# Kernel tuning notes

Measured on AMD Instinct MI355X. Metric: run time of the kernel, lower is better.

## Reference

```python
import jax, jax.numpy as jnp
import numpy as np

N = 100_000      # atoms
E = 1_600_000    # edges (avg degree 16)
B = 50           # graphs in batch
H = 128          # hidden dim
R = 50           # num radial features (emb(0.0, 6.0, 50))
MAXZ = 100
CUTOFF = 6.0
L = 3            # interaction layers (ext[1..6])


def setup_inputs() -> dict:
    key = jax.random.key(0)
    ks = jax.random.split(key, 16)
    z = jax.random.randint(ks[0], (N,), 0, MAXZ)
    pos = jax.random.normal(ks[1], (N, 3), dtype=jnp.float32) * 3.0
    cell = jnp.eye(3, dtype=jnp.float32)[None] * 10.0 + 0.1 * jax.random.normal(ks[2], (B, 3, 3), dtype=jnp.float32)
    edge_index = jax.random.randint(ks[3], (2, E), 0, N)
    cell_offsets = jax.random.randint(ks[4], (E, 3), -1, 2)  # {-1,0,1}
    edge_batch = jax.random.randint(ks[5], (E,), 0, B)
    # learned parameters
    atom_emb = jax.random.normal(ks[6], (MAXZ, H), dtype=jnp.float32) * 0.1
    dist_table = jax.random.normal(ks[7], (R, R), dtype=jnp.float32) * 0.1  # dist_emb embedding table
    s_e = 1.0 / np.sqrt(2 * H + R)
    s_h = 1.0 / np.sqrt(H)
    We = jax.random.normal(ks[8], (L, 2 * H + R, H), dtype=jnp.float32) * s_e
    be = jnp.zeros((L, H), dtype=jnp.float32)
    Wv = jax.random.normal(ks[9], (L, H, H), dtype=jnp.float32) * s_h
    bv = jnp.zeros((L, H), dtype=jnp.float32)
    Wh = jax.random.normal(ks[10], (H, H), dtype=jnp.float32) * s_h
    bh = jnp.zeros((H,), dtype=jnp.float32)
    return dict(z=z, pos=pos, cell=cell, edge_index=edge_index,
                cell_offsets=cell_offsets, edge_batch=edge_batch,
                atom_emb=atom_emb, dist_table=dist_table,
                We=We, be=be, Wv=Wv, bv=bv, Wh=Wh, bh=bh)


def reference(z, pos, cell, edge_index, cell_offsets, edge_batch,
              atom_emb, dist_table, We, be, Wv, bv, Wh, bh):
    row, col = edge_index[0], edge_index[1]
    # get_pbc_distances: offsets = cell_offsets @ per-edge cell
    off = jnp.einsum('ek,ekl->el', cell_offsets.astype(jnp.float32), cell[edge_batch])  # [E,3]
    vec = pos[row] - pos[col] + off
    dist = jnp.sqrt(jnp.sum(vec * vec, axis=-1))  # [E]
    # dist_emb(dist.to(long)): integer-cast distance indexes the embedding table
    demb = dist_table[jnp.clip(dist.astype(jnp.int32), 0, R - 1)]  # [E,R]
    env = 0.5 * (jnp.cos(jnp.pi * jnp.clip(dist, 0.0, CUTOFF) / CUTOFF) + 1.0)  # cosine cutoff [E]
    v = atom_emb[z]  # ext[0]: atom embedding [N,H]
    for i in range(L):
        # ext[2i+1]: edge layer — gather endpoints, concat with radial features
        m = jnp.concatenate([v[row], v[col], demb], axis=-1)  # [E, 2H+R]
        e = jax.nn.silu(m @ We[i] + be[i]) * env[:, None]     # [E, H]
        # ext[2i+2]: node layer — scatter-sum messages to destination nodes
        agg = jax.ops.segment_sum(e, col, num_segments=N)     # [N, H]
        v = v + jax.nn.silu(agg @ Wv[i] + bv[i])
    v = v @ Wh + bh  # head
    return (v, pos, dist)
```

## Files before the change

kernel.cpp:

```cpp
#include <hip/hip_runtime.h>
#include <hip/hip_bf16.h>

#define HID 128
#define RR 50
#define NLAY 3
#define CBSH 9
#define CBSZ 512
#define CPAD (CBSZ * 3)
#define ACHUNK 8192

typedef __attribute__((ext_vector_type(8))) short short8;
typedef __attribute__((ext_vector_type(4))) float f32x4;
typedef __attribute__((ext_vector_type(2))) float f32x2;

static __device__ __forceinline__ unsigned short f2bf(float x) {
    unsigned int b = __builtin_bit_cast(unsigned int, x);
    b = b + 0x7FFFu + ((b >> 16) & 1u);
    return (unsigned short)(b >> 16);
}
static __device__ __forceinline__ float bf2f(unsigned int u) {
    return __builtin_bit_cast(float, u << 16);
}
static __device__ __forceinline__ f32x2 bfpair(unsigned u) {
    f32x2 r;
    r.x = __builtin_bit_cast(float, u << 16);
    r.y = __builtin_bit_cast(float, u & 0xffff0000u);
    return r;
}
static __device__ __forceinline__ float silu_f(float x) {
    float e = __expf(-x);
    return x * __builtin_amdgcn_rcpf(1.0f + e);
}

__global__ __launch_bounds__(256) void k_geom(
    const int* __restrict__ ei, const int* __restrict__ co,
    const int* __restrict__ eb, const float* __restrict__ cell,
    const float* __restrict__ pos, float* __restrict__ dist_out,
    int2* __restrict__ rec, int* __restrict__ ccol,
    float* __restrict__ out_pos, int* __restrict__ gb,
    int N3, int E, int nCB)
{
    __shared__ int lc[1024];
    int tid = threadIdx.x;
    for (int i = tid; i < 1024; i += 256) lc[i] = 0;
    __syncthreads();
    int e = blockIdx.x * 256 + tid;
    if (e < N3) out_pos[e] = pos[e];
    if (e < E) {
        int r = ei[e], c = ei[E + e], b = eb[e];
        float c0 = (float)co[3*e], c1 = (float)co[3*e+1], c2 = (float)co[3*e+2];
        const float* cb = cell + b * 9;
        float v0 = pos[3*r+0] - pos[3*c+0] + c0*cb[0] + c1*cb[3] + c2*cb[6];
        float v1 = pos[3*r+1] - pos[3*c+1] + c0*cb[1] + c1*cb[4] + c2*cb[7];
        float v2 = pos[3*r+2] - pos[3*c+2] + c0*cb[2] + c1*cb[5] + c2*cb[8];
        float d = sqrtf(v0*v0 + v1*v1 + v2*v2);
        dist_out[e] = d;
        bool keep = d < 6.0f;
        ccol[e] = keep ? c : -1;
        if (keep) {
            int di = (int)d;
            di = di < 0 ? 0 : (di > RR - 1 ? RR - 1 : di);
            float envv = 0.5f * (cosf(d * (3.14159265358979323846f / 6.0f)) + 1.0f);
            rec[e] = make_int2((r << 8) | di, __builtin_bit_cast(int, envv));
            atomicAdd(&lc[((unsigned)c) >> CBSH], 1);
        }
    }
    __syncthreads();
    for (int i = tid; i < nCB; i += 256)
        if (lc[i]) atomicAdd(&gb[i], lc[i]);
}

__global__ __launch_bounds__(256) void k_projz(
    const int* __restrict__ z, const float* __restrict__ emb,
    const unsigned short* __restrict__ P12t,
    unsigned short* __restrict__ v, unsigned short* __restrict__ P1,
    unsigned short* __restrict__ P2, int N)
{
    int gid = blockIdx.x * 256 + threadIdx.x;
    if (gid >= N * 16) return;
    int n = gid >> 4, c4 = gid & 15;
    int zz = z[n];
    const float4* ep = (const float4*)(emb + (size_t)zz * HID) + c4 * 2;
    float4 a = ep[0], b = ep[1];
    uint4 u;
    u.x = ((unsigned)f2bf(a.y) << 16) | f2bf(a.x);
    u.y = ((unsigned)f2bf(a.w) << 16) | f2bf(a.z);
    u.z = ((unsigned)f2bf(b.y) << 16) | f2bf(b.x);
    u.w = ((unsigned)f2bf(b.w) << 16) | f2bf(b.z);
    *(uint4*)(v + (size_t)n * HID + c4 * 8) = u;
    uint4 t1 = *(const uint4*)(P12t + (size_t)zz * 256 + c4 * 8);
    uint4 t2 = *(const uint4*)(P12t + (size_t)zz * 256 + 128 + c4 * 8);
    *(uint4*)(P1 + (size_t)n * HID + c4 * 8) = t1;
    *(uint4*)(P2 + (size_t)n * HID + c4 * 8) = t2;
}

__global__ __launch_bounds__(256) void k_wprep(
    const float* __restrict__ We, const float* __restrict__ Wv,
    const float* __restrict__ Wh, const float* __restrict__ dt,
    const float* __restrict__ be, const float* __restrict__ emb,
    unsigned short* __restrict__ WvP, unsigned short* __restrict__ WcP,
    unsigned short* __restrict__ WhP, unsigned short* __restrict__ TbP,
    unsigned short* __restrict__ P12t)
{
    int blk = blockIdx.x;
    if (blk < 640) {
        int t = blk * 256 + threadIdx.x;
        int j = t & 7, l = (t >> 3) & 63, s = (t >> 9) & 3;
        int ln = l & 15, g = l >> 4;
        int k = s * 32 + g * 4 + (j & 3) + ((j >> 2) << 4);
        if (t < 3 * 16384) {
            int i = t >> 14; int nt = (t >> 11) & 7;
            WvP[t] = f2bf(Wv[(size_t)i * 16384 + k * HID + nt * 16 + ln]);
        } else if (t < 3 * 16384 + 3 * 32768) {
            int u = t - 3 * 16384; int i = u >> 15; int nt = (u >> 11) & 15;
            int col = nt * 16 + ln;
            float val = (col < HID) ? We[(size_t)i * 306 * HID + k * HID + col]
                                    : We[(size_t)i * 306 * HID + (HID + k) * HID + (col - HID)];
            WcP[u] = f2bf(val);
        } else {
            int u = t - 3 * 16384 - 3 * 32768; int nt = (u >> 11) & 7;
            WhP[u] = f2bf(Wh[k * HID + nt * 16 + ln]);
        }
    } else if (blk < 640 + NLAY * RR) {
        if (threadIdx.x >= HID) return;
        int row = blk - 640;
        int i = row / RR, r = row % RR;
        int c = threadIdx.x;
        float s = be[i * HID + c];
        const float* w = We + (size_t)i * 306 * HID + 256 * HID + c;
        const float* dr = dt + r * RR;
        for (int k = 0; k < RR; ++k) s += dr[k] * w[k * HID];
        TbP[(i * RR + r) * HID + c] = f2bf(s);
    } else {
        int zz = blk - 640 - NLAY * RR;
        int c = threadIdx.x;
        int cm = c & 127, half = c >> 7;
        const float* er = emb + (size_t)zz * HID;
        const float* w = We + (size_t)(half * 128) * HID + cm;
        float s = 0.f;
        #pragma unroll 8
        for (int k = 0; k < 128; ++k) s += er[k] * w[k * HID];
        P12t[(size_t)zz * 256 + c] = f2bf(s);
    }
}

__global__ __launch_bounds__(256) void k_scanA(
    const int* __restrict__ gb, int* __restrict__ gbase,
    int* __restrict__ gcur, int nCB)
{
    __shared__ int ps[256];
    __shared__ int carry;
    int t = threadIdx.x;
    if (t == 0) carry = 0;
    __syncthreads();
    for (int base = 0; base < nCB; base += 256) {
        int v = (base + t < nCB) ? gb[base + t] : 0;
        ps[t] = v; __syncthreads();
        for (int d = 1; d < 256; d <<= 1) {
            int x = (t >= d) ? ps[t - d] : 0;
            __syncthreads();
            ps[t] += x;
            __syncthreads();
        }
        int excl = carry + ps[t] - v;
        if (base + t < nCB) { gbase[base + t] = excl; gcur[base + t] = excl; }
        __syncthreads();
        if (t == 0) carry += ps[255];
        __syncthreads();
    }
    if (t == 0) gbase[nCB] = carry;
}

__global__ __launch_bounds__(256) void k_splitA(
    const int* __restrict__ col, const int2* __restrict__ rec,
    int* __restrict__ gcur, int2* __restrict__ binned,
    int* __restrict__ bcol, int E, int nCB)
{
    __shared__ int lc[1024];
    __shared__ int lres[1024];
    int tid = threadIdx.x;
    for (int i = tid; i < nCB; i += 256) lc[i] = 0;
    __syncthreads();
    int base = blockIdx.x * ACHUNK;
    int end = base + ACHUNK; if (end > E) end = E;
    for (int e = base + tid; e < end; e += 256) {
        int c = col[e];
        if (c >= 0) atomicAdd(&lc[((unsigned)c) >> CBSH], 1);
    }
    __syncthreads();
    for (int i = tid; i < nCB; i += 256) {
        lres[i] = lc[i] ? atomicAdd(&gcur[i], lc[i]) : 0;
        lc[i] = 0;
    }
    __syncthreads();
    for (int e = base + tid; e < end; e += 256) {
        int c = col[e];
        if (c < 0) continue;
        int b = ((unsigned)c) >> CBSH;
        int rank = atomicAdd(&lc[b], 1);
        int p = lres[b] + rank;
        binned[p] = rec[e];
        bcol[p] = c;
    }
}

__global__ __launch_bounds__(256) void k_sortB(
    const int2* __restrict__ binned, const int* __restrict__ bcol,
    const int* __restrict__ gbase, int2* __restrict__ meta,
    int2* __restrict__ noff, int N)
{
    __shared__ int lcnt[CBSZ], lcur[CBSZ], pscan[CBSZ];
    __shared__ int wsum[64];
    const int b = blockIdx.x;
    const int tid = threadIdx.x;
    const int s = gbase[b], e = gbase[b + 1];
    const int mbase = s + b * CPAD;
    for (int i = tid; i < CBSZ; i += 256) { lcnt[i] = 0; lcur[i] = 0; }
    __syncthreads();
    for (int t = s + tid; t < e; t += 256)
        atomicAdd(&lcnt[bcol[t] & (CBSZ - 1)], 1);
    __syncthreads();
    if (tid < 64) {
        int ssum = 0;
        #pragma unroll
        for (int k = 0; k < 8; ++k) {
            int idx = tid * 8 + k;
            int pc = (lcnt[idx] + 3) & ~3;
            pscan[idx] = ssum;
            ssum += pc;
        }
        wsum[tid] = ssum;
    }
    __syncthreads();
    if (tid == 0) {
        int c = 0;
        for (int i = 0; i < 64; ++i) { int t = wsum[i]; wsum[i] = c; c += t; }
    }
    __syncthreads();
    if (tid < 64) {
        #pragma unroll
        for (int k = 0; k < 8; ++k) pscan[tid * 8 + k] += wsum[tid];
    }
    __syncthreads();
    for (int i = tid; i < CBSZ; i += 256) {
        int node = (b << CBSH) + i;
        if (node < N) {
            noff[node] = make_int2(mbase + pscan[i], lcnt[i]);
            int pb = mbase + pscan[i] + lcnt[i];
            int pads = ((lcnt[i] + 3) & ~3) - lcnt[i];
            for (int k = 0; k < pads; ++k) meta[pb + k] = make_int2(0, 0);
        }
    }
    __syncthreads();
    for (int t = s + tid; t < e; t += 256) {
        int local = bcol[t] & (CBSZ - 1);
        int rank = atomicAdd(&lcur[local], 1);
        meta[mbase + pscan[local] + rank] = binned[t];
    }
}

#define PLD(M) (*(const unsigned*)(P1b + (unsigned)((((unsigned)(M).x) & 0xFFFFFF00u) | lane4)))
#define TLDG(M) (*(const unsigned*)(Tb_ + (((((unsigned)(M).x) & 255u) << 8) | lane4)))

#define EP(GG, TBU, MM)                                                       \
    {                                                                         \
        f32x2 xx = bfpair(GG) + (bfpair(TBU) + p2v);                          \
        f32x2 nx = xx * -1.442695041f;                                        \
        f32x2 ee;                                                             \
        ee.x = __builtin_amdgcn_exp2f(nx.x);                                  \
        ee.y = __builtin_amdgcn_exp2f(nx.y);                                  \
        f32x2 dd = ee + 1.0f;                                                 \
        f32x2 rr;                                                             \
        rr.x = __builtin_amdgcn_rcpf(dd.x);                                   \
        rr.y = __builtin_amdgcn_rcpf(dd.y);                                   \
        f32x2 sl = xx * rr;                                                   \
        float evf = __builtin_bit_cast(float, (MM).y);                        \
        av += sl * evf;                                                       \
    }

static __device__ __forceinline__ short8 ldfrag(const unsigned short* A, int r, int s, int g) {
    const char* p = (const char*)(A + r * 136) + s * 64 + g * 8;
    uint2 lo = *(const uint2*)p;
    uint2 hi = *(const uint2*)(p + 32);
    uint4 u; u.x = lo.x; u.y = lo.y; u.z = hi.x; u.w = hi.y;
    return __builtin_bit_cast(short8, u);
}

template<int NT2, bool FINAL>
__global__ __launch_bounds__(512) void k_layer(
    const unsigned short* __restrict__ P1,
    const unsigned short* __restrict__ P2,
    const unsigned short* __restrict__ TbBf,
    const int2* __restrict__ meta,
    const int2* __restrict__ noff,
    const unsigned short* __restrict__ B1p,
    const float* __restrict__ b1,
    unsigned short* __restrict__ v,
    const unsigned short* __restrict__ B2p,
    const float* __restrict__ b2,
    unsigned short* __restrict__ P1d,
    unsigned short* __restrict__ P2d,
    float* __restrict__ outd, int N)
{
    __shared__ __align__(16) unsigned short SHB[2 * 32 * 136];
    unsigned short* SH  = SHB;
    unsigned short* SHV = SHB + 32 * 136;
    const int tid = threadIdx.x;
    const int node0 = blockIdx.x * 32;
    const int w = tid >> 6, l = tid & 63, g = (l >> 4) & 3, ln = l & 15;
    const int lane = l;
    const unsigned lane4 = 4u * (unsigned)lane;

    {
        int r = tid >> 4, c = tid & 15;
        uint4 y4 = make_uint4(0, 0, 0, 0);
        if (node0 + r < N) y4 = *(const uint4*)(v + (size_t)(node0 + r) * HID + c * 8);
        *(uint4*)(SHV + r * 136 + c * 8) = y4;
    }

    {
        const char* P1b = (const char*)P1;
        const char* Tb_ = (const char*)TbBf;
        const int r0 = w << 2;
        int2 ni = make_int2(0, 0);
        {
            int pn = node0 + r0 + lane;
            if (lane < 4 && pn < N) ni = noff[pn];
        }
        #pragma unroll 1
        for (int i = 0; i < 4; ++i) {
            int r = r0 + i;
            unsigned* outp = (unsigned*)(SH + r * 136 + 2 * lane);
            int n = __builtin_amdgcn_readlane(ni.y, i);
            if (n == 0) { *outp = 0u; continue; }
            int s = __builtin_amdgcn_readlane(ni.x, i);
            int node = node0 + r;
            unsigned p2u = *(const unsigned*)(P2 + (size_t)node * HID + 2 * lane);
            n = (n + 3) & ~3;
            f32x2 p2v = bfpair(p2u);
            f32x2 av; av.x = 0.f; av.y = 0.f;
            const int2* mp = meta + s;
            int2 m0 = mp[0], m1 = mp[1], m2 = mp[2], m3 = mp[3];
            unsigned g0 = PLD(m0), g1 = PLD(m1), g2 = PLD(m2), g3 = PLD(m3);
            for (int t = 0; t < n; t += 4) {
                int2 n0 = mp[t + 4], n1 = mp[t + 5], n2 = mp[t + 6], n3 = mp[t + 7];
                unsigned h0 = PLD(n0), h1 = PLD(n1), h2 = PLD(n2), h3 = PLD(n3);
                unsigned t0 = TLDG(m0), t1 = TLDG(m1), t2 = TLDG(m2), t3 = TLDG(m3);
                EP(g0, t0, m0) EP(g1, t1, m1) EP(g2, t2, m2) EP(g3, t3, m3)
                m0 = n0; m1 = n1; m2 = n2; m3 = n3;
                g0 = h0; g1 = h1; g2 = h2; g3 = h3;
            }
            *outp = (((unsigned)f2bf(av.y)) << 16) | (unsigned)f2bf(av.x);
        }
    }

    {
        short8 bf1[4];
        #pragma unroll
        for (int s = 0; s < 4; ++s)
            bf1[s] = *(const short8*)(B1p + ((w * 4 + s) * 64 + l) * 8);
        __syncthreads();
        f32x4 acc[2] = {};
        #pragma unroll
        for (int s = 0; s < 4; ++s)
            #pragma unroll
            for (int mt = 0; mt < 2; ++mt) {
                short8 af = ldfrag(SH, 16 * mt + ln, s, g);
                acc[mt] = __builtin_amdgcn_mfma_f32_16x16x32_bf16(af, bf1[s], acc[mt], 0, 0, 0);
            }
        __syncthreads();
        float bvc = b1[16 * w + ln];
        #pragma unroll
        for (int mt = 0; mt < 2; ++mt) {
            int col = 16 * w + ln;
            #pragma unroll
            for (int j = 0; j < 4; ++j) {
                int r = 16 * mt + 4 * g + j;
                float y = silu_f(acc[mt][j] + bvc);
                float vn = bf2f((unsigned)SHV[r * 136 + col]) + y;
                SH[r * 136 + col] = f2bf(vn);
            }
        }
        __syncthreads();
        if (!FINAL) {
            int r = tid >> 4, c = tid & 15;
            if (node0 + r < N)
                *(uint4*)(v + (size_t)(node0 + r) * HID + c * 8) =
                    *(const uint4*)(SH + r * 136 + c * 8);
        }
    }

    constexpr int NTW = NT2 / 8;
    short8 bf2[NTW][4];
    #pragma unroll
    for (int nt = 0; nt < NTW; ++nt)
        #pragma unroll
        for (int s = 0; s < 4; ++s)
            bf2[nt][s] = *(const short8*)(B2p + (((w * NTW + nt) * 4 + s) * 64 + l) * 8);
    f32x4 acc2[2][NTW] = {};
    #pragma unroll
    for (int s = 0; s < 4; ++s)
        #pragma unroll
        for (int mt = 0; mt < 2; ++mt) {
            short8 af = ldfrag(SH, 16 * mt + ln, s, g);
            #pragma unroll
            for (int nt = 0; nt < NTW; ++nt)
                acc2[mt][nt] = __builtin_amdgcn_mfma_f32_16x16x32_bf16(af, bf2[nt][s], acc2[mt][nt], 0, 0, 0);
        }
    __syncthreads();
    if (FINAL) {
        float* fst = (float*)SHB;
        int col = w * 16 + ln;
        float bb = b2[col];
        #pragma unroll
        for (int mt = 0; mt < 2; ++mt)
            #pragma unroll
            for (int j = 0; j < 4; ++j) {
                int r = 16 * mt + 4 * g + j;
                fst[r * 132 + col] = acc2[mt][0][j] + bb;
            }
        __syncthreads();
        #pragma unroll
        for (int i = 0; i < 2; ++i) {
            int u = tid + 512 * i, r = u >> 5, cg = u & 31;
            if (node0 + r < N)
                *(float4*)(outd + (size_t)(node0 + r) * HID + cg * 4) =
                    *(const float4*)(fst + r * 132 + cg * 4);
        }
    } else {
        #pragma unroll
        for (int nt = 0; nt < NTW; ++nt) {
            int gidx = w * NTW + nt;
            int colm = (gidx * 16 + ln) & 127;
            unsigned short* dst = (gidx < 8) ? SHV : SH;
            #pragma unroll
            for (int mt = 0; mt < 2; ++mt)
                #pragma unroll
                for (int j = 0; j < 4; ++j) {
                    int r = 16 * mt + 4 * g + j;
                    dst[r * 136 + colm] = f2bf(acc2[mt][nt][j]);
                }
        }
        __syncthreads();
        {
            int r = tid >> 4, cg = tid & 15;
            if (node0 + r < N) {
                *(uint4*)(P1d + (size_t)(node0 + r) * HID + cg * 8) =
                    *(const uint4*)(SHV + r * 136 + cg * 8);
                *(uint4*)(P2d + (size_t)(node0 + r) * HID + cg * 8) =
                    *(const uint4*)(SH + r * 136 + cg * 8);
            }
        }
    }
}

extern "C" void kernel_launch(void* const* d_in, const int* in_sizes, int n_in,
                              void* d_out, int out_size, void* d_ws, size_t ws_size,
                              hipStream_t stream)
{
    const int*   z    = (const int*)d_in[0];
    const float* pos  = (const float*)d_in[1];
    const float* cell = (const float*)d_in[2];
    const int*   ei   = (const int*)d_in[3];
    const int*   co   = (const int*)d_in[4];
    const int*   eb   = (const int*)d_in[5];
    const float* emb  = (const float*)d_in[6];
    const float* dt   = (const float*)d_in[7];
    const float* We   = (const float*)d_in[8];
    const float* be   = (const float*)d_in[9];
    const float* Wv   = (const float*)d_in[10];
    const float* bv   = (const float*)d_in[11];
    const float* Wh   = (const float*)d_in[12];
    const float* bh   = (const float*)d_in[13];

    const int N = in_sizes[0];
    const int E = in_sizes[5];
    const int MAXZ = in_sizes[6] / HID;
    const int nCB = (N + CBSZ - 1) >> CBSH;
    const size_t metaN = (size_t)E + (size_t)nCB * CPAD + 32;

    char* p = (char*)d_ws;
    unsigned short* v    = (unsigned short*)p;  p += (size_t)N * HID * 2;
    unsigned short* P1a  = (unsigned short*)p;  p += (size_t)N * HID * 2;
    unsigned short* P1b  = (unsigned short*)p;  p += (size_t)N * HID * 2;
    unsigned short* P2   = (unsigned short*)p;  p += (size_t)N * HID * 2;
    int2*  meta  = (int2*)p;                    p += metaN * 8;
    int2*  noff  = (int2*)p;                    p += (size_t)N * 8;
    int*   gb    = (int*)p;                     p += (size_t)(nCB + 1) * 4;
    int*   gbase = (int*)p;                     p += (size_t)(nCB + 1) * 4;
    int*   gcur  = (int*)p;                     p += (size_t)(nCB + 1) * 4;
    unsigned short* TbP = (unsigned short*)p;   p += (size_t)NLAY * RR * HID * 2;
    unsigned short* WvP = (unsigned short*)p;   p += (size_t)3 * 16384 * 2;
    unsigned short* WcP = (unsigned short*)p;   p += (size_t)3 * 32768 * 2;
    unsigned short* WhP = (unsigned short*)p;   p += (size_t)16384 * 2;
    unsigned short* P12t = (unsigned short*)p;  p += (size_t)MAXZ * 256 * 2;

    int2* rec    = (int2*)P1a;
    int2* binned = (int2*)((char*)P1a + (size_t)E * 8);
    int*  ccol   = (int*)P2;
    int*  bcol   = (int*)((char*)P2 + (size_t)E * 4);

    float* out_v    = (float*)d_out;
    float* out_pos  = out_v + (size_t)N * HID;
    float* out_dist = out_pos + (size_t)N * 3;

    const int nlayer = (N + 31) / 32;
    const int nblkA = (E + ACHUNK - 1) / ACHUNK;
    const int N3 = N * 3;
    int ngeom = (E + 255) / 256;
    if ((N3 + 255) / 256 > ngeom) ngeom = (N3 + 255) / 256;

    hipMemsetAsync(gb, 0, (size_t)(nCB + 1) * 4, stream);
    hipMemsetAsync(meta, 0, metaN * 8, stream);
    k_geom<<<ngeom, 256, 0, stream>>>(ei, co, eb, cell, pos, out_dist, rec, ccol,
                                      out_pos, gb, N3, E, nCB);
    k_scanA<<<1, 256, 0, stream>>>(gb, gbase, gcur, nCB);
    k_splitA<<<nblkA, 256, 0, stream>>>(ccol, rec, gcur, binned, bcol, E, nCB);
    k_sortB<<<nCB, 256, 0, stream>>>(binned, bcol, gbase, meta, noff, N);

    k_wprep<<<640 + NLAY * RR + MAXZ, 256, 0, stream>>>(
        We, Wv, Wh, dt, be, emb, WvP, WcP, WhP, TbP, P12t);

    k_projz<<<(N * 16 + 255) / 256, 256, 0, stream>>>(z, emb, P12t, v, P1a, P2, N);

    unsigned short* Pin  = P1a;
    unsigned short* Pout = P1b;
    for (int i = 0; i < NLAY; ++i) {
        if (i < NLAY - 1) {
            k_layer<16, false><<<nlayer, 512, 0, stream>>>(
                Pin, P2, TbP + (size_t)i * RR * HID, meta, noff,
                WvP + (size_t)i * 16384, bv + (size_t)i * HID, v,
                WcP + (size_t)(i + 1) * 32768, nullptr, Pout, P2, nullptr, N);
        } else {
            k_layer<8, true><<<nlayer, 512, 0, stream>>>(
                Pin, P2, TbP + (size_t)i * RR * HID, meta, noff,
                WvP + (size_t)i * 16384, bv + (size_t)i * HID, v,
                WhP, bh, nullptr, nullptr, out_v, N);
        }
        unsigned short* t = Pin; Pin = Pout; Pout = t;
    }
}
```

Before: 246.7 us.

## Fuse atom-embedding init into first layer and use global atomics in geometry

The first layer kernel now builds the bf16 node state straight from the atom embedding table and reads the P2 projection from the per-species table. k_projz therefore writes only P1, and the N×H v and P2 initial writes and their reads go away. k_geom drops its shared-memory bucket histogram and does one global atomicAdd per kept edge, which removes two block barriers but adds heavy global atomic contention on about 200 counters.

Measured after the change: 257.6 us. 4.4% more time.

```diff
diff --git a/kernel.cpp b/kernel.cpp
--- a/kernel.cpp
+++ b/kernel.cpp
@@ -37,61 +37,40 @@
     const int* __restrict__ eb, const float* __restrict__ cell,
     const float* __restrict__ pos, float* __restrict__ dist_out,
     int2* __restrict__ rec, int* __restrict__ ccol,
-    float* __restrict__ out_pos, int* __restrict__ gb,
-    int N3, int E, int nCB)
-{
-    __shared__ int lc[1024];
-    int tid = threadIdx.x;
-    for (int i = tid; i < 1024; i += 256) lc[i] = 0;
-    __syncthreads();
-    int e = blockIdx.x * 256 + tid;
+    float* __restrict__ out_pos, int* __restrict__ gb, int N3, int E)
+{
+    int e = blockIdx.x * 256 + threadIdx.x;
     if (e < N3) out_pos[e] = pos[e];
-    if (e < E) {
-        int r = ei[e], c = ei[E + e], b = eb[e];
-        float c0 = (float)co[3*e], c1 = (float)co[3*e+1], c2 = (float)co[3*e+2];
-        const float* cb = cell + b * 9;
-        float v0 = pos[3*r+0] - pos[3*c+0] + c0*cb[0] + c1*cb[3] + c2*cb[6];
-        float v1 = pos[3*r+1] - pos[3*c+1] + c0*cb[1] + c1*cb[4] + c2*cb[7];
-        float v2 = pos[3*r+2] - pos[3*c+2] + c0*cb[2] + c1*cb[5] + c2*cb[8];
-        float d = sqrtf(v0*v0 + v1*v1 + v2*v2);
-        dist_out[e] = d;
-        bool keep = d < 6.0f;
-        ccol[e] = keep ? c : -1;
-        if (keep) {
-            int di = (int)d;
-            di = di < 0 ? 0 : (di > RR - 1 ? RR - 1 : di);
-            float envv = 0.5f * (cosf(d * (3.14159265358979323846f / 6.0f)) + 1.0f);
-            rec[e] = make_int2((r << 8) | di, __builtin_bit_cast(int, envv));
-            atomicAdd(&lc[((unsigned)c) >> CBSH], 1);
-        }
-    }
-    __syncthreads();
-    for (int i = tid; i < nCB; i += 256)
-        if (lc[i]) atomicAdd(&gb[i], lc[i]);
+    if (e >= E) return;
+    int r = ei[e], c = ei[E + e], b = eb[e];
+    float c0 = (float)co[3*e], c1 = (float)co[3*e+1], c2 = (float)co[3*e+2];
+    const float* cb = cell + b * 9;
+    float v0 = pos[3*r+0] - pos[3*c+0] + c0*cb[0] + c1*cb[3] + c2*cb[6];
+    float v1 = pos[3*r+1] - pos[3*c+1] + c0*cb[1] + c1*cb[4] + c2*cb[7];
+    float v2 = pos[3*r+2] - pos[3*c+2] + c0*cb[2] + c1*cb[5] + c2*cb[8];
+    float d = sqrtf(v0*v0 + v1*v1 + v2*v2);
+    dist_out[e] = d;
+    bool keep = d < 6.0f;
+    ccol[e] = keep ? c : -1;
+    if (keep) {
+        int di = (int)d;
+        di = di < 0 ? 0 : (di > RR - 1 ? RR - 1 : di);
+        float envv = 0.5f * (cosf(d * (3.14159265358979323846f / 6.0f)) + 1.0f);
+        rec[e] = make_int2((r << 8) | di, __builtin_bit_cast(int, envv));
+        atomicAdd(&gb[((unsigned)c) >> CBSH], 1);
+    }
 }
 
 __global__ __launch_bounds__(256) void k_projz(
-    const int* __restrict__ z, const float* __restrict__ emb,
-    const unsigned short* __restrict__ P12t,
-    unsigned short* __restrict__ v, unsigned short* __restrict__ P1,
-    unsigned short* __restrict__ P2, int N)
+    const int* __restrict__ z, const unsigned short* __restrict__ P12t,
+    unsigned short* __restrict__ P1, int N)
 {
     int gid = blockIdx.x * 256 + threadIdx.x;
     if (gid >= N * 16) return;
     int n = gid >> 4, c4 = gid & 15;
     int zz = z[n];
-    const float4* ep = (const float4*)(emb + (size_t)zz * HID) + c4 * 2;
-    float4 a = ep[0], b = ep[1];
-    uint4 u;
-    u.x = ((unsigned)f2bf(a.y) << 16) | f2bf(a.x);
-    u.y = ((unsigned)f2bf(a.w) << 16) | f2bf(a.z);
-    u.z = ((unsigned)f2bf(b.y) << 16) | f2bf(b.x);
-    u.w = ((unsigned)f2bf(b.w) << 16) | f2bf(b.z);
-    *(uint4*)(v + (size_t)n * HID + c4 * 8) = u;
     uint4 t1 = *(const uint4*)(P12t + (size_t)zz * 256 + c4 * 8);
-    uint4 t2 = *(const uint4*)(P12t + (size_t)zz * 256 + 128 + c4 * 8);
     *(uint4*)(P1 + (size_t)n * HID + c4 * 8) = t1;
-    *(uint4*)(P2 + (size_t)n * HID + c4 * 8) = t2;
 }
 
 __global__ __launch_bounds__(256) void k_wprep(
@@ -286,13 +265,16 @@
     return __builtin_bit_cast(short8, u);
 }
 
-template<int NT2, bool FINAL>
+template<int NT2, bool FINAL, bool FIRST>
 __global__ __launch_bounds__(512) void k_layer(
     const unsigned short* __restrict__ P1,
     const unsigned short* __restrict__ P2,
     const unsigned short* __restrict__ TbBf,
     const int2* __restrict__ meta,
     const int2* __restrict__ noff,
+    const int* __restrict__ z,
+    const float* __restrict__ emb,
+    const unsigned short* __restrict__ P12t,
     const unsigned short* __restrict__ B1p,
     const float* __restrict__ b1,
     unsigned short* __restrict__ v,
@@ -314,7 +296,19 @@
     {
         int r = tid >> 4, c = tid & 15;
         uint4 y4 = make_uint4(0, 0, 0, 0);
-        if (node0 + r < N) y4 = *(const uint4*)(v + (size_t)(node0 + r) * HID + c * 8);
+        if (node0 + r < N) {
+            if (FIRST) {
+                int zz = z[node0 + r];
+                const float4* ep = (const float4*)(emb + (size_t)zz * HID) + c * 2;
+                float4 a = ep[0], b = ep[1];
+                y4.x = ((unsigned)f2bf(a.y) << 16) | f2bf(a.x);
+                y4.y = ((unsigned)f2bf(a.w) << 16) | f2bf(a.z);
+                y4.z = ((unsigned)f2bf(b.y) << 16) | f2bf(b.x);
+                y4.w = ((unsigned)f2bf(b.w) << 16) | f2bf(b.z);
+            } else {
+                y4 = *(const uint4*)(v + (size_t)(node0 + r) * HID + c * 8);
+            }
+        }
         *(uint4*)(SHV + r * 136 + c * 8) = y4;
     }
 
@@ -323,9 +317,13 @@
         const char* Tb_ = (const char*)TbBf;
         const int r0 = w << 2;
         int2 ni = make_int2(0, 0);
+        int zq = 0;
         {
             int pn = node0 + r0 + lane;
-            if (lane < 4 && pn < N) ni = noff[pn];
+            if (lane < 4 && pn < N) {
+                ni = noff[pn];
+                if (FIRST) zq = z[pn];
+            }
         }
         #pragma unroll 1
         for (int i = 0; i < 4; ++i) {
@@ -335,7 +333,13 @@
             if (n == 0) { *outp = 0u; continue; }
             int s = __builtin_amdgcn_readlane(ni.x, i);
             int node = node0 + r;
-            unsigned p2u = *(const unsigned*)(P2 + (size_t)node * HID + 2 * lane);
+            unsigned p2u;
+            if (FIRST) {
+                int zz = __builtin_amdgcn_readlane(zq, i);
+                p2u = *(const unsigned*)(P12t + (size_t)zz * 256 + 128 + 2 * lane);
+            } else {
+                p2u = *(const unsigned*)(P2 + (size_t)node * HID + 2 * lane);
+            }
             n = (n + 3) & ~3;
             f32x2 p2v = bfpair(p2u);
             f32x2 av; av.x = 0.f; av.y = 0.f;
@@ -513,7 +517,7 @@
     hipMemsetAsync(gb, 0, (size_t)(nCB + 1) * 4, stream);
     hipMemsetAsync(meta, 0, metaN * 8, stream);
     k_geom<<<ngeom, 256, 0, stream>>>(ei, co, eb, cell, pos, out_dist, rec, ccol,
-                                      out_pos, gb, N3, E, nCB);
+                                      out_pos, gb, N3, E);
     k_scanA<<<1, 256, 0, stream>>>(gb, gbase, gcur, nCB);
     k_splitA<<<nblkA, 256, 0, stream>>>(ccol, rec, gcur, binned, bcol, E, nCB);
     k_sortB<<<nCB, 256, 0, stream>>>(binned, bcol, gbase, meta, noff, N);
@@ -521,22 +525,17 @@
     k_wprep<<<640 + NLAY * RR + MAXZ, 256, 0, stream>>>(
         We, Wv, Wh, dt, be, emb, WvP, WcP, WhP, TbP, P12t);
 
-    k_projz<<<(N * 16 + 255) / 256, 256, 0, stream>>>(z, emb, P12t, v, P1a, P2, N);
-
-    unsigned short* Pin  = P1a;
-    unsigned short* Pout = P1b;
-    for (int i = 0; i < NLAY; ++i) {
-        if (i < NLAY - 1) {
-            k_layer<16, false><<<nlayer, 512, 0, stream>>>(
-                Pin, P2, TbP + (size_t)i * RR * HID, meta, noff,
-                WvP + (size_t)i * 16384, bv + (size_t)i * HID, v,
-                WcP + (size_t)(i + 1) * 32768, nullptr, Pout, P2, nullptr, N);
-        } else {
-            k_layer<8, true><<<nlayer, 512, 0, stream>>>(
-                Pin, P2, TbP + (size_t)i * RR * HID, meta, noff,
-                WvP + (size_t)i * 16384, bv + (size_t)i * HID, v,
-                WhP, bh, nullptr, nullptr, out_v, N);
-        }
-        unsigned short* t = Pin; Pin = Pout; Pout = t;
-    }
-}
+    k_projz<<<(N * 16 + 255) / 256, 256, 0, stream>>>(z, P12t, P1a, N);
+
+    k_layer<16, false, true><<<nlayer, 512, 0, stream>>>(
+        P1a, nullptr, TbP, meta, noff, z, emb, P12t,
+        WvP, bv, v, WcP + (size_t)32768, nullptr, P1b, P2, nullptr, N);
+    k_layer<16, false, false><<<nlayer, 512, 0, stream>>>(
+        P1b, P2, TbP + (size_t)RR * HID, meta, noff, nullptr, nullptr, nullptr,
+        WvP + (size_t)16384, bv + (size_t)HID, v,
+        WcP + (size_t)2 * 32768, nullptr, P1a, P2, nullptr, N);
+    k_layer<8, true, false><<<nlayer, 512, 0, stream>>>(
+        P1a, P2, TbP + (size_t)2 * RR * HID, meta, noff, nullptr, nullptr, nullptr,
+        WvP + (size_t)2 * 16384, bv + (size_t)2 * HID, v,
+        WhP, bh, nullptr, nullptr, out_v, N);
+}
```
